# Kernel tuning notes

Hardware: AMD Instinct MI355X
Metric: run time of the kernel (lower is better)

The kernel has to match this reference:

```python
import jax, jax.numpy as jnp
import numpy as np
import math

H = 1024      # hidden_size
NH = 16       # num_attention_heads
HD = H // NH  # head_dim = 64
FF = 4096     # intermediate_size
AD = 256      # adapter_hidden_size
NB = 320      # num_buckets
MAXD = 800    # max_bucket_distance
B = 4
S = 1024
EPS = 1e-5


def _rel_bucket(rel):
    # HF WavLM _relative_positions_bucket
    nb = NB // 2
    buckets = (rel > 0).astype(jnp.int32) * nb
    rel = jnp.abs(rel)
    max_exact = nb // 2
    is_small = rel < max_exact
    large = max_exact + (
        jnp.log(jnp.maximum(rel, 1).astype(jnp.float32) / max_exact)
        / math.log(MAXD / max_exact) * (nb - max_exact)
    ).astype(jnp.int32)
    large = jnp.minimum(large, nb - 1)
    return buckets + jnp.where(is_small, rel, large)


def _ln(x, g, b):
    m = x.mean(-1, keepdims=True)
    v = ((x - m) ** 2).mean(-1, keepdims=True)
    return (x - m) * jax.lax.rsqrt(v + EPS) * g + b


def setup_inputs() -> dict:
    key = jax.random.key(0)
    ks = jax.random.split(key, 12)
    sc = 0.02
    w = lambda k, shape: jax.random.normal(k, shape, jnp.float32) * sc
    return dict(
        x=jax.random.normal(ks[0], (B, S, H), jnp.float32),
        Wq=w(ks[1], (H, H)), bq=jnp.zeros((H,), jnp.float32),
        Wk=w(ks[2], (H, H)), bk=jnp.zeros((H,), jnp.float32),
        Wv=w(ks[3], (H, H)), bv=jnp.zeros((H,), jnp.float32),
        Wo=w(ks[4], (H, H)), bo=jnp.zeros((H,), jnp.float32),
        Wg=w(ks[5], (8, HD)), bg=jnp.zeros((8,), jnp.float32),
        gru_const=jnp.ones((1, NH, 1, 1), jnp.float32),
        rel_embed=w(ks[6], (NB, NH)),
        ln1_g=jnp.ones((H,), jnp.float32), ln1_b=jnp.zeros((H,), jnp.float32),
        W1=w(ks[7], (FF, H)), b1=jnp.zeros((FF,), jnp.float32),
        W2=w(ks[8], (H, FF)), b2=jnp.zeros((H,), jnp.float32),
        ln2_g=jnp.ones((H,), jnp.float32), ln2_b=jnp.zeros((H,), jnp.float32),
        Wad=w(ks[9], (AD, H)), bad=jnp.zeros((AD,), jnp.float32),
        Wau=w(ks[10], (H, AD)), bau=jnp.zeros((H,), jnp.float32),
    )


def reference(x, Wq, bq, Wk, bk, Wv, bv, Wo, bo, Wg, bg, gru_const, rel_embed,
              ln1_g, ln1_b, W1, b1, W2, b2, ln2_g, ln2_b, Wad, bad, Wau, bau):
    b, s, _ = x.shape
    # --- relative position bias (first layer: position_bias=None) ---
    pos = jnp.arange(s)
    rel = pos[None, :] - pos[:, None]                 # memory - context
    pos_bias = rel_embed[_rel_bucket(rel)].transpose(2, 0, 1)  # (nh, s, s)

    # --- GRU-style gating of the bias (per batch, head, query pos) ---
    xh = x.reshape(b, s, NH, HD).transpose(0, 2, 1, 3)         # (b, nh, s, hd)
    gproj = jnp.einsum('bhsd,ed->bhse', xh, Wg) + bg           # (b, nh, s, 8)
    gproj = gproj.reshape(b, NH, s, 2, 4).sum(-1)              # (b, nh, s, 2)
    gate = jax.nn.sigmoid(gproj)
    gate_a, gate_b = gate[..., 0:1], gate[..., 1:2]            # (b, nh, s, 1)
    gate_out = gate_a * (gate_b * gru_const - 1.0) + 2.0       # (b, nh, s, 1)
    gated_bias = gate_out * pos_bias[None]                     # (b, nh, s, s)

    # --- multi-head self-attention with additive gated bias ---
    q = (x @ Wq.T + bq).reshape(b, s, NH, HD)
    k = (x @ Wk.T + bk).reshape(b, s, NH, HD)
    v = (x @ Wv.T + bv).reshape(b, s, NH, HD)
    scores = jnp.einsum('bihd,bjhd->bhij', q, k) * (HD ** -0.5) + gated_bias
    attn = jax.nn.softmax(scores, axis=-1)
    ctx = jnp.einsum('bhij,bjhd->bihd', attn, v).reshape(b, s, H)
    attn_out = ctx @ Wo.T + bo

    # --- residual + LN, FFN + adapter (idx_without_adapter=None path) + LN ---
    h = _ln(x + attn_out, ln1_g, ln1_b)
    ff = jax.nn.gelu(h @ W1.T + b1, approximate=False) @ W2.T + b2
    adapt = jax.nn.elu(h @ Wad.T + bad) @ Wau.T + bau
    h = h + ff + adapt
    return _ln(h, ln2_g, ln2_b)
```

## Files before the change

kernel.cpp:

```cpp
#include <hip/hip_runtime.h>
#include <cmath>

typedef unsigned short u16;
using short8 = __attribute__((ext_vector_type(8))) short;
using f32x4  = __attribute__((ext_vector_type(4))) float;

__device__ __forceinline__ u16 f2bf(float f) {
  union { float f; unsigned u; } c; c.f = f;
  unsigned r = c.u + 0x7fffu + ((c.u >> 16) & 1u);
  return (u16)(r >> 16);
}
__device__ __forceinline__ float bf2f(u16 b) {
  union { unsigned u; float f; } c; c.u = ((unsigned)b) << 16;
  return c.f;
}

__device__ __forceinline__ void gld_lds16(void* lds, const void* g) {
  __builtin_amdgcn_global_load_lds(
      (const __attribute__((address_space(1))) void*)g,
      (__attribute__((address_space(3))) void*)lds, 16, 0, 0);
}

__device__ __forceinline__ float gelu_fast(float t) {
  float u = 0.7978845608f * t * (1.f + 0.044715f * t * t);
  float th = 1.f - 2.f / (__expf(2.f * u) + 1.f);
  return 0.5f * t * (1.f + th);
}

__global__ __launch_bounds__(256) void cvt_bf16(const float* __restrict__ in,
                                                u16* __restrict__ out, int n4) {
  int i = blockIdx.x * 256 + threadIdx.x;
  if (i >= n4) return;
  float4 v = ((const float4*)in)[i];
  ushort4 o;
  o.x = f2bf(v.x); o.y = f2bf(v.y); o.z = f2bf(v.z); o.w = f2bf(v.w);
  ((ushort4*)out)[i] = o;
}

__global__ __launch_bounds__(256) void cvt_pad(const float* __restrict__ in,
                                               u16* __restrict__ out,
                                               int incols4, int outstride, int n4) {
  int i = blockIdx.x * 256 + threadIdx.x;
  if (i >= n4) return;
  int row = i / incols4, c = i - row * incols4;
  float4 v = ((const float4*)in)[i];
  ushort4 o;
  o.x = f2bf(v.x); o.y = f2bf(v.y); o.z = f2bf(v.z); o.w = f2bf(v.w);
  *(ushort4*)&out[(size_t)row * outstride + c * 4] = o;
}

__global__ __launch_bounds__(256) void btab_kernel(const float* __restrict__ rel_embed,
                                                   float* __restrict__ btab) {
  int idx = blockIdx.x * 256 + threadIdx.x;
  if (idx >= 16 * 2048) return;
  int h = idx >> 11;
  int d = idx & 2047;
  if (d >= 2047) return;
  int rel = d - 1023;
  int bucket = (rel > 0) ? 160 : 0;
  int ar = rel < 0 ? -rel : rel;
  if (ar < 80) {
    bucket += ar;
  } else {
    int large = 80 + (int)(logf((float)ar / 80.0f) / 2.3025851f * 80.0f);
    if (large > 159) large = 159;
    bucket += large;
  }
  btab[h * 2048 + d] = rel_embed[bucket * 16 + h];
}

__global__ __launch_bounds__(256) void gate_kernel(const float* __restrict__ x,
                                                   const float* __restrict__ Wg,
                                                   const float* __restrict__ bg,
                                                   const float* __restrict__ gc,
                                                   float* __restrict__ gate_out) {
  int gw = blockIdx.x * 4 + (threadIdx.x >> 6);
  int lane = threadIdx.x & 63;
  int s = gw & 1023, bh = gw >> 10, b = bh >> 4, h = bh & 15;
  float wA = Wg[lane] + Wg[64 + lane] + Wg[128 + lane] + Wg[192 + lane];
  float wB = Wg[256 + lane] + Wg[320 + lane] + Wg[384 + lane] + Wg[448 + lane];
  float xv = x[((size_t)(b * 1024 + s)) * 1024 + h * 64 + lane];
  float pa = xv * wA, pb = xv * wB;
  #pragma unroll
  for (int m = 1; m < 64; m <<= 1) {
    pa += __shfl_xor(pa, m, 64);
    pb += __shfl_xor(pb, m, 64);
  }
  if (lane == 0) {
    float bgA = bg[0] + bg[1] + bg[2] + bg[3];
    float bgB = bg[4] + bg[5] + bg[6] + bg[7];
    float ga = 1.f / (1.f + expf(-(pa + bgA)));
    float gb = 1.f / (1.f + expf(-(pb + bgB)));
    gate_out[(size_t)bh * 1024 + s] = ga * (gb * gc[h] - 1.f) + 2.f;
  }
}

__global__ __launch_bounds__(256) void vtrans_kernel(const u16* __restrict__ vb,
                                                     u16* __restrict__ vt) {
  __shared__ u16 tile[64 * 65];
  int bh = blockIdx.y, b = bh >> 4, h = bh & 15;
  int s0 = blockIdx.x * 64;
  int tid = threadIdx.x;
  int r = tid >> 3, c = (tid & 7) * 8;
  #pragma unroll
  for (int p = 0; p < 2; ++p) {
    int s = p * 32 + r;
    uint4 vv = *(const uint4*)&vb[((size_t)(b * 1024 + s0 + s)) * 1024 + h * 64 + c];
    const u16* pv = (const u16*)&vv;
    #pragma unroll
    for (int e = 0; e < 8; ++e) tile[(c + e) * 65 + s] = pv[e];
  }
  __syncthreads();
  int d = tid & 63, jc0 = tid >> 6;
  #pragma unroll
  for (int jc = jc0; jc < 8; jc += 4) {
    u16 tmp[8];
    #pragma unroll
    for (int e = 0; e < 8; ++e) tmp[e] = tile[d * 65 + jc * 8 + e];
    *(uint4*)&vt[((size_t)(bh * 64 + d)) * 1024 + s0 + jc * 8] = *(uint4*)tmp;
  }
}

template <int MODE>
__global__ __launch_bounds__(256, 3) void gemm_bt(
    const u16* __restrict__ A, const u16* __restrict__ Bw,
    int K, int Ksub, int N, int bn0,
    const float* __restrict__ bias0, const float* __restrict__ bias1,
    const float* __restrict__ bias2,
    float* __restrict__ outf,
    u16* __restrict__ ob0, u16* __restrict__ ob1, u16* __restrict__ ob2) {
  __shared__ __align__(16) u16 As[3][128 * 32];
  __shared__ __align__(16) u16 Bs[3][128 * 32];
  const int tid = threadIdx.x;
  const int lane = tid & 63, wave = tid >> 6;
  const int quad = lane >> 4, l16 = lane & 15;
  const int bm = blockIdx.x * 128, bn = blockIdx.y * 128;
  const int kz = blockIdx.z;
  const int nsteps = Ksub >> 5;
  const int wm = (wave & 1) * 64, wn = (wave >> 1) * 64;
  const int sr = lane & 15, skc = (lane >> 4) * 8;

  const u16* a0 = A + (size_t)(bm + wave * 32 + sr) * K + kz * Ksub + skc;
  const u16* b0 = Bw + (size_t)(bn + wave * 32 + sr) * K + kz * Ksub + skc;
  const size_t ra = (size_t)16 * K;

  f32x4 acc[4][4] = {};

  #pragma unroll
  for (int t = 0; t < 2; ++t) {
    gld_lds16(&As[0][(wave * 2 + t) * 512], a0 + t * ra);
    gld_lds16(&Bs[0][(wave * 2 + t) * 512], b0 + t * ra);
  }
  if (nsteps > 1) {
    #pragma unroll
    for (int t = 0; t < 2; ++t) {
      gld_lds16(&As[1][(wave * 2 + t) * 512], a0 + t * ra + 32);
      gld_lds16(&Bs[1][(wave * 2 + t) * 512], b0 + t * ra + 32);
    }
  }

  int cur = 0, nxt2 = 2;
  for (int ks = 0; ks < nsteps; ++ks) {
    if (ks + 1 < nsteps) asm volatile("s_waitcnt vmcnt(4)" ::: "memory");
    else                 asm volatile("s_waitcnt vmcnt(0)" ::: "memory");
    __builtin_amdgcn_s_barrier();
    if (ks + 2 < nsteps) {
      int ko = (ks + 2) * 32;
      #pragma unroll
      for (int t = 0; t < 2; ++t) {
        gld_lds16(&As[nxt2][(wave * 2 + t) * 512], a0 + t * ra + ko);
        gld_lds16(&Bs[nxt2][(wave * 2 + t) * 512], b0 + t * ra + ko);
      }
    }
    const u16* Ap = As[cur];
    const u16* Bp = Bs[cur];
    short8 af[4], bf[4];
    #pragma unroll
    for (int mi = 0; mi < 4; ++mi)
      af[mi] = *(const short8*)&Ap[((wm >> 4) + mi) * 512 + quad * 128 + l16 * 8];
    #pragma unroll
    for (int ni = 0; ni < 4; ++ni)
      bf[ni] = *(const short8*)&Bp[((wn >> 4) + ni) * 512 + quad * 128 + l16 * 8];
    #pragma unroll
    for (int mi = 0; mi < 4; ++mi)
      #pragma unroll
      for (int ni = 0; ni < 4; ++ni)
        acc[mi][ni] = __builtin_amdgcn_mfma_f32_16x16x32_bf16(af[mi], bf[ni], acc[mi][ni], 0, 0, 0);
    cur = (cur == 2) ? 0 : cur + 1;
    nxt2 = (nxt2 == 2) ? 0 : nxt2 + 1;
  }

  float* outp = outf + (size_t)kz * 4194304;

  #pragma unroll
  for (int mi = 0; mi < 4; ++mi) {
    #pragma unroll
    for (int ni = 0; ni < 4; ++ni) {
      int col = bn + bn0 + wn + ni * 16 + l16;
      #pragma unroll
      for (int r = 0; r < 4; ++r) {
        int m = bm + wm + mi * 16 + quad * 4 + r;
        float v = acc[mi][ni][r];
        if constexpr (MODE == 0) {
          int seg = col >> 10;
          int nloc = col & 1023;
          const float* bs = seg == 0 ? bias0 : (seg == 1 ? bias1 : bias2);
          u16* dst = seg == 0 ? ob0 : (seg == 1 ? ob1 : ob2);
          v += bs[nloc];
          if (seg == 0) v *= 0.125f;
          dst[(size_t)m * 1024 + nloc] = f2bf(v);
        } else if constexpr (MODE == 2) {
          if (col < 4096) {
            float t = v + bias0[col];
            ob0[(size_t)m * 4352 + col] = f2bf(gelu_fast(t));
          } else {
            float t = v + bias1[col - 4096];
            float e = t > 0.f ? t : (__expf(t) - 1.f);
            ob0[(size_t)m * 4352 + col] = f2bf(e);
          }
        } else {
          outp[(size_t)m * N + col] = v;
        }
      }
    }
  }
}

#define VMCNT(n) asm volatile("s_waitcnt vmcnt(" #n ")" ::: "memory")
#define NOOPST ((void)0)

#define G256_LDA(BUF, KK, MH)                                               \
  af_[0] = *(const short8*)&lds[BUF][0][KK][aBase + (MH) * 2048 + 0];       \
  af_[1] = *(const short8*)&lds[BUF][0][KK][aBase + (MH) * 2048 + 512];     \
  af_[2] = *(const short8*)&lds[BUF][0][KK][aBase + (MH) * 2048 + 1024];    \
  af_[3] = *(const short8*)&lds[BUF][0][KK][aBase + (MH) * 2048 + 1536];
#define G256_LDB(BUF, KK)                                                   \
  bf_[0] = *(const short8*)&lds[BUF][1][KK][bBase + 0];                     \
  bf_[1] = *(const short8*)&lds[BUF][1][KK][bBase + 512];                   \
  bf_[2] = *(const short8*)&lds[BUF][1][KK][bBase + 1024];                  \
  bf_[3] = *(const short8*)&lds[BUF][1][KK][bBase + 1536];
#define G256_MFMA(MH)                                                       \
  _Pragma("unroll") for (int mi = 0; mi < 4; ++mi)                          \
  _Pragma("unroll") for (int ni = 0; ni < 4; ++ni)                          \
    acc[(MH) * 4 + mi][ni] = __builtin_amdgcn_mfma_f32_16x16x32_bf16(       \
        af_[mi], bf_[ni], acc[(MH) * 4 + mi][ni], 0, 0, 0);
#define G256_PHASE(BUF, KK, MH, DOB, STAGE, WAIT)                           \
  {                                                                         \
    G256_LDA(BUF, KK, MH)                                                   \
    if (DOB) { G256_LDB(BUF, KK) }                                          \
    STAGE;                                                                  \
    __builtin_amdgcn_s_barrier();                                           \
    asm volatile("s_waitcnt lgkmcnt(0)" ::: "memory");                      \
    __builtin_amdgcn_s_setprio(1);                                          \
    G256_MFMA(MH)                                                           \
    __builtin_amdgcn_s_setprio(0);                                          \
    WAIT;                                                                   \
    __builtin_amdgcn_s_barrier();                                           \
  }

template <int MODE>
__global__ __launch_bounds__(512, 2) void gemm256(
    const u16* __restrict__ A, const u16* __restrict__ Bw,
    int lda, int ldb, int kt_hi, int kt_lo, int z_hi,
    const float* __restrict__ bias0, const float* __restrict__ bias1,
    const float* __restrict__ bias2,
    float* __restrict__ outf, float* __restrict__ outf2, int ldo,
    u16* __restrict__ ob0, u16* __restrict__ ob1, u16* __restrict__ ob2) {
  __shared__ __align__(16) u16 lds[2][2][2][8192];

  const int tid = threadIdx.x;
  const int lane = tid & 63, wave = tid >> 6;
  const int quad = lane >> 4, l16 = lane & 15;
  const int wm = wave >> 2, wn = wave & 3;

  const int gx = gridDim.x, gy = gridDim.y;
  int flat = blockIdx.x + gx * (blockIdx.y + gy * blockIdx.z);
  const int cpx = (gx * gy * gridDim.z) >> 3;
  flat = (flat & 7) * cpx + (flat >> 3);
  const int bmi = flat % gx;
  int rest = flat / gx;
  const int bni = rest % gy;
  const int kz = rest / gy;

  const int bm = bmi * 256, bn = bni * 256;
  const int nkt = (kz < z_hi) ? kt_hi : kt_lo;
  const int ktb = (kz < z_hi) ? kz * kt_hi : z_hi * kt_hi + (kz - z_hi) * kt_lo;
  const int nIter = nkt >> 1;

  const int srow = wave * 16 + (lane >> 2);
  const int sk = (((lane & 3) ^ ((lane >> 3) & 3)) << 3);
  const u16* aG = A + (size_t)(bm + srow) * lda + (size_t)ktb * 64 + sk;
  const u16* bG = Bw + (size_t)(bn + srow) * ldb + (size_t)ktb * 64 + sk;
  const size_t aS = (size_t)128 * lda, bS = (size_t)128 * ldb;

  const int xsw = ((quad ^ ((l16 >> 1) & 3)) << 3);
  const int aBase = (wm * 128 + l16) * 32 + xsw;
  const int bBase = (wn * 64 + l16) * 32 + xsw;

  auto stA = [&](int buf, int kh, int kt) {
    const u16* g = aG + kt * 64 + kh * 32;
    u16* d = (u16*)&lds[buf][0][kh][wave * 512];
    gld_lds16(d, g);
    gld_lds16(d + 4096, g + aS);
  };
  auto stB = [&](int buf, int kh, int kt) {
    const u16* g = bG + kt * 64 + kh * 32;
    u16* d = (u16*)&lds[buf][1][kh][wave * 512];
    gld_lds16(d, g);
    gld_lds16(d + 4096, g + bS);
  };

  f32x4 acc[8][4] = {};
  short8 af_[4], bf_[4];

  stA(0, 0, 0); stB(0, 0, 0); stA(0, 1, 0); stB(0, 1, 0);
  stA(1, 0, 1); stB(1, 0, 1);
  VMCNT(0);
  __builtin_amdgcn_s_barrier();

  for (int J = 0; J < nIter - 1; ++J) {
    const int o = 2 * J + 1, e = 2 * J + 2, on = 2 * J + 3;
    G256_PHASE(0, 0, 0, 1, stA(1, 1, o),  NOOPST)
    G256_PHASE(0, 0, 1, 0, stB(1, 1, o),  VMCNT(8))
    G256_PHASE(0, 1, 0, 1, stA(0, 0, e),  NOOPST)
    G256_PHASE(0, 1, 1, 0, stB(0, 0, e),  VMCNT(8))
    G256_PHASE(1, 0, 0, 1, stA(0, 1, e),  NOOPST)
    G256_PHASE(1, 0, 1, 0, stB(0, 1, e),  VMCNT(8))
    G256_PHASE(1, 1, 0, 1, stA(1, 0, on), NOOPST)
    G256_PHASE(1, 1, 1, 0, stB(1, 0, on), VMCNT(8))
  }
  {
    const int o = nkt - 1;
    G256_PHASE(0, 0, 0, 1, stA(1, 1, o), NOOPST)
    G256_PHASE(0, 0, 1, 0, stB(1, 1, o), NOOPST)
    G256_PHASE(0, 1, 0, 1, NOOPST,       NOOPST)
    G256_PHASE(0, 1, 1, 0, NOOPST,       VMCNT(4))
    G256_PHASE(1, 0, 0, 1, NOOPST,       NOOPST)
    G256_PHASE(1, 0, 1, 0, NOOPST,       VMCNT(0))
    G256_PHASE(1, 1, 0, 1, NOOPST,       NOOPST)
    G256_PHASE(1, 1, 1, 0, NOOPST,       NOOPST)
  }

  const int m0 = bm + wm * 128 + quad * 4;
  const int n0 = bn + wn * 64 + l16;

  if constexpr (MODE == 0) {
    const int seg = bn >> 10;
    const float* bs = seg == 0 ? bias0 : (seg == 1 ? bias1 : bias2);
    u16* dst = seg == 0 ? ob0 : (seg == 1 ? ob1 : ob2);
    const float sc = seg == 0 ? 0.125f : 1.0f;
    const int nb = (bn & 1023) + wn * 64 + l16;
    #pragma unroll
    for (int a = 0; a < 8; ++a)
      #pragma unroll
      for (int ni = 0; ni < 4; ++ni) {
        int nn = nb + ni * 16;
        float bv = bs[nn];
        #pragma unroll
        for (int r = 0; r < 4; ++r) {
          int m = m0 + a * 16 + r;
          dst[(size_t)m * 1024 + nn] = f2bf((acc[a][ni][r] + bv) * sc);
        }
      }
  } else if constexpr (MODE == 2) {
    #pragma unroll
    for (int a = 0; a < 8; ++a)
      #pragma unroll
      for (int ni = 0; ni < 4; ++ni) {
        int nn = n0 + ni * 16;
        float bv = bias0[nn];
        #pragma unroll
        for (int r = 0; r < 4; ++r) {
          int m = m0 + a * 16 + r;
          ob0[(size_t)m * 4352 + nn] = f2bf(gelu_fast(acc[a][ni][r] + bv));
        }
      }
  } else {
    float* op = (kz < 2) ? outf + (size_t)kz * 4194304
                         : outf2 + (size_t)(kz - 2) * 4194304;
    #pragma unroll
    for (int a = 0; a < 8; ++a)
      #pragma unroll
      for (int ni = 0; ni < 4; ++ni) {
        int nn = n0 + ni * 16;
        #pragma unroll
        for (int r = 0; r < 4; ++r)
          op[(size_t)(m0 + a * 16 + r) * ldo + nn] = acc[a][ni][r];
      }
  }
}

__global__ __launch_bounds__(256) void attn_kernel(
    const u16* __restrict__ qb, const u16* __restrict__ kb, const u16* __restrict__ vt,
    const float* __restrict__ gate, const float* __restrict__ btab,
    u16* __restrict__ ctxb) {
  __shared__ __align__(16) u16 Qs[64 * 64];
  __shared__ __align__(16) u16 Ks[64 * 64];
  __shared__ __align__(16) u16 Vs[64 * 64];
  __shared__ __align__(16) u16 Ps[4][16 * 64];
  __shared__ u16 btl[2048];
  __shared__ float gbuf[64];

  const int tid = threadIdx.x;
  const int lane = tid & 63, wave = tid >> 6;
  const int quad = lane >> 4, l16 = lane & 15;
  const int it0 = blockIdx.x * 64;
  const int bh = blockIdx.y, b = bh >> 4, h = bh & 15;
  const int sr = lane & 15;
  const int skc = (lane >> 4) * 8;

  for (int idx = tid; idx < 2047; idx += 256) btl[idx] = f2bf(btab[h * 2048 + idx]);
  if (tid < 64) gbuf[tid] = gate[(size_t)bh * 1024 + it0 + tid];

  #pragma unroll
  for (int hf = 0; hf < 2; ++hf)
    gld_lds16(&Qs[wave * 1024 + hf * 512],
              &qb[((size_t)(b * 1024 + it0 + wave * 16 + sr)) * 1024 + h * 64 + hf * 32 + skc]);

  f32x4 oacc[4] = {};
  float mrow[4], lrow[4];
  #pragma unroll
  for (int r = 0; r < 4; ++r) { mrow[r] = -1e30f; lrow[r] = 0.f; }

  __syncthreads();

  for (int jt = 0; jt < 16; ++jt) {
    int j0 = jt * 64;
    #pragma unroll
    for (int hf = 0; hf < 2; ++hf) {
      gld_lds16(&Ks[wave * 1024 + hf * 512],
                &kb[((size_t)(b * 1024 + j0 + wave * 16 + sr)) * 1024 + h * 64 + hf * 32 + skc]);
      gld_lds16(&Vs[wave * 1024 + hf * 512],
                &vt[((size_t)(bh * 64 + wave * 16 + sr)) * 1024 + j0 + hf * 32 + skc]);
    }
    __syncthreads();

    f32x4 sacc[4] = {};
    #pragma unroll
    for (int c = 0; c < 2; ++c) {
      short8 aq = *(const short8*)&Qs[wave * 1024 + (c * 4 + quad) * 128 + l16 * 8];
      #pragma unroll
      for (int nt = 0; nt < 4; ++nt) {
        short8 bk8 = *(const short8*)&Ks[nt * 1024 + (c * 4 + quad) * 128 + l16 * 8];
        sacc[nt] = __builtin_amdgcn_mfma_f32_16x16x32_bf16(aq, bk8, sacc[nt], 0, 0, 0);
      }
    }

    float sc[4][4], mt[4];
    #pragma unroll
    for (int r = 0; r < 4; ++r) {
      int i_loc = wave * 16 + quad * 4 + r;
      int i_glob = it0 + i_loc;
      float g = gbuf[i_loc];
      float mx = -1e30f;
      #pragma unroll
      for (int nt = 0; nt < 4; ++nt) {
        int j = j0 + nt * 16 + l16;
        float s = sacc[nt][r] + g * bf2f(btl[j - i_glob + 1023]);
        sc[nt][r] = s;
        mx = fmaxf(mx, s);
      }
      mt[r] = mx;
    }
    #pragma unroll
    for (int m = 1; m < 16; m <<= 1)
      #pragma unroll
      for (int r = 0; r < 4; ++r) mt[r] = fmaxf(mt[r], __shfl_xor(mt[r], m, 64));

    float alpha[4], ls[4];
    #pragma unroll
    for (int r = 0; r < 4; ++r) {
      float mnew = fmaxf(mrow[r], mt[r]);
      alpha[r] = __expf(mrow[r] - mnew);
      mrow[r] = mnew;
      float lsum = 0.f;
      #pragma unroll
      for (int nt = 0; nt < 4; ++nt) {
        float p = __expf(sc[nt][r] - mnew);
        sc[nt][r] = p;
        lsum += p;
      }
      ls[r] = lsum;
    }
    #pragma unroll
    for (int m = 1; m < 16; m <<= 1)
      #pragma unroll
      for (int r = 0; r < 4; ++r) ls[r] += __shfl_xor(ls[r], m, 64);
    #pragma unroll
    for (int r = 0; r < 4; ++r) lrow[r] = lrow[r] * alpha[r] + ls[r];

    #pragma unroll
    for (int nt = 0; nt < 4; ++nt)
      #pragma unroll
      for (int r = 0; r < 4; ++r)
        Ps[wave][(nt * 2 + (l16 >> 3)) * 128 + (quad * 4 + r) * 8 + (l16 & 7)] = f2bf(sc[nt][r]);

    #pragma unroll
    for (int dt = 0; dt < 4; ++dt)
      #pragma unroll
      for (int r = 0; r < 4; ++r) oacc[dt][r] *= alpha[r];

    #pragma unroll
    for (int c = 0; c < 2; ++c) {
      short8 ap = *(const short8*)&Ps[wave][(c * 4 + quad) * 128 + l16 * 8];
      #pragma unroll
      for (int dt = 0; dt < 4; ++dt) {
        short8 bv8 = *(const short8*)&Vs[dt * 1024 + (c * 4 + quad) * 128 + l16 * 8];
        oacc[dt] = __builtin_amdgcn_mfma_f32_16x16x32_bf16(ap, bv8, oacc[dt], 0, 0, 0);
      }
    }
    __syncthreads();
  }

  #pragma unroll
  for (int dt = 0; dt < 4; ++dt)
    #pragma unroll
    for (int r = 0; r < 4; ++r) {
      int i_loc = wave * 16 + quad * 4 + r;
      int d = dt * 16 + l16;
      float o = oacc[dt][r] / lrow[r];
      ctxb[((size_t)(b * 1024 + it0 + i_loc)) * 1024 + h * 64 + d] = f2bf(o);
    }
}

template <bool WRITE_BF16, bool TWO_BIAS, int NP>
__global__ __launch_bounds__(256) void redln_kernel(
    const float* __restrict__ p0, const float* __restrict__ p1,
    const float* __restrict__ p2, const float* __restrict__ p3,
    const float* __restrict__ extra, const float* __restrict__ bias,
    const float* __restrict__ bias2,
    const float* __restrict__ g, const float* __restrict__ bta,
    float* __restrict__ outf, u16* __restrict__ outb) {
  __shared__ float red[8];
  int row = blockIdx.x, tid = threadIdx.x;
  int lane = tid & 63, wave = tid >> 6;
  size_t base = (size_t)row * 1024 + tid * 4;
  float4 a = *(const float4*)&p0[base];
  float4 bb = *(const float4*)&p1[base];
  float4 c = *(const float4*)&extra[base];
  float4 d = *(const float4*)&bias[tid * 4];
  float4 v;
  v.x = a.x + bb.x + c.x + d.x;
  v.y = a.y + bb.y + c.y + d.y;
  v.z = a.z + bb.z + c.z + d.z;
  v.w = a.w + bb.w + c.w + d.w;
  if (NP == 4) {
    float4 e2 = *(const float4*)&p2[base];
    float4 e3 = *(const float4*)&p3[base];
    v.x += e2.x + e3.x; v.y += e2.y + e3.y;
    v.z += e2.z + e3.z; v.w += e2.w + e3.w;
  }
  if (TWO_BIAS) {
    float4 d2 = *(const float4*)&bias2[tid * 4];
    v.x += d2.x; v.y += d2.y; v.z += d2.z; v.w += d2.w;
  }
  float s = v.x + v.y + v.z + v.w;
  #pragma unroll
  for (int m = 1; m < 64; m <<= 1) s += __shfl_xor(s, m, 64);
  if (lane == 0) red[wave] = s;
  __syncthreads();
  float mean = (red[0] + red[1] + red[2] + red[3]) * (1.f / 1024.f);
  float d0 = v.x - mean, d1 = v.y - mean, d2 = v.z - mean, d3 = v.w - mean;
  float sq = d0 * d0 + d1 * d1 + d2 * d2 + d3 * d3;
  #pragma unroll
  for (int m = 1; m < 64; m <<= 1) sq += __shfl_xor(sq, m, 64);
  if (lane == 0) red[4 + wave] = sq;
  __syncthreads();
  float var = (red[4] + red[5] + red[6] + red[7]) * (1.f / 1024.f);
  float rstd = rsqrtf(var + 1e-5f);
  float dd[4] = {d0, d1, d2, d3};
  #pragma unroll
  for (int e = 0; e < 4; ++e) {
    int cidx = tid * 4 + e;
    float val = dd[e] * rstd * g[cidx] + bta[cidx];
    outf[(size_t)row * 1024 + cidx] = val;
    if (WRITE_BF16) outb[(size_t)row * 1024 + cidx] = f2bf(val);
  }
}

extern "C" void kernel_launch(void* const* d_in, const int* in_sizes, int n_in,
                              void* d_out, int out_size, void* d_ws, size_t ws_size,
                              hipStream_t stream) {
  const float* x    = (const float*)d_in[0];
  const float* Wq   = (const float*)d_in[1];  const float* bq  = (const float*)d_in[2];
  const float* Wk   = (const float*)d_in[3];  const float* bk  = (const float*)d_in[4];
  const float* Wv   = (const float*)d_in[5];  const float* bv  = (const float*)d_in[6];
  const float* Wo   = (const float*)d_in[7];  const float* bo  = (const float*)d_in[8];
  const float* Wg   = (const float*)d_in[9];  const float* bg  = (const float*)d_in[10];
  const float* gc   = (const float*)d_in[11];
  const float* rel  = (const float*)d_in[12];
  const float* ln1g = (const float*)d_in[13]; const float* ln1b = (const float*)d_in[14];
  const float* W1   = (const float*)d_in[15]; const float* b1  = (const float*)d_in[16];
  const float* W2   = (const float*)d_in[17]; const float* b2  = (const float*)d_in[18];
  const float* ln2g = (const float*)d_in[19]; const float* ln2b = (const float*)d_in[20];
  const float* Wad  = (const float*)d_in[21]; const float* bad = (const float*)d_in[22];
  const float* Wau  = (const float*)d_in[23]; const float* bau = (const float*)d_in[24];
  float* out = (float*)d_out;

  char* ws = (char*)d_ws;
  const size_t MB = 1ull << 20;
  const size_t KB = 1ull << 10;
  (void)n_in; (void)in_sizes; (void)out_size;

  const bool big = ws_size >= (135ull << 20);

  u16 *xb, *wqkv, *qb, *kb, *vbp, *vtb, *ctxb, *wob, *w1ad, *w2au, *ffadp, *hb;
  float *gate, *btab, *P0, *P1, *P2, *P3, *hf;
  xb    = (u16*)(ws + 0 * MB);
  wqkv  = (u16*)(ws + 8 * MB);
  ffadp = (u16*)(ws + 0 * MB);
  P0    = (float*)(ws + 34 * MB);
  P1    = (float*)(ws + 50 * MB);
  if (big) {
    P2   = (float*)(ws + 66 * MB);
    P3   = (float*)(ws + 82 * MB);
    qb   = (u16*)(ws + 66 * MB);
    kb   = (u16*)(ws + 74 * MB);
    vbp  = (u16*)(ws + 82 * MB);
    vtb  = (u16*)(ws + 90 * MB);
    hb   = (u16*)(ws + 82 * MB);
    ctxb = (u16*)(ws + 98 * MB);
    hf   = (float*)(ws + 98 * MB);
    wob  = (u16*)(ws + 114 * MB);
    w1ad = (u16*)(ws + 116 * MB);
    w2au = (u16*)(ws + 125 * MB);
    gate = (float*)(ws + 133 * MB + 512 * KB);
    btab = (float*)(ws + 133 * MB + 768 * KB);
  } else {
    P2   = P0;  P3 = P0;
    qb   = (u16*)(ws + 14 * MB);
    kb   = (u16*)(ws + 22 * MB);
    vbp  = (u16*)(ws + 30 * MB);
    vtb  = (u16*)(ws + 38 * MB);
    gate = (float*)(ws + 46 * MB);
    btab = (float*)(ws + 46 * MB + 256 * KB);
    ctxb = (u16*)(ws + 66 * MB);
    wob  = (u16*)(ws + 74 * MB);
    w1ad = (u16*)(ws + 76 * MB);
    w2au = (u16*)(ws + 85 * MB);
    hf   = (float*)(ws + 94 * MB);
    hb   = (u16*)(ws + 110 * MB);
  }

  auto cvt = [&](const float* src, u16* dst, int n) {
    cvt_bf16<<<(n / 4 + 255) / 256, 256, 0, stream>>>(src, dst, n / 4);
  };
  cvt(x, xb, 4096 * 1024);
  cvt(Wq, wqkv,               1024 * 1024);
  cvt(Wk, wqkv + 1024 * 1024, 1024 * 1024);
  cvt(Wv, wqkv + 2 * 1024 * 1024, 1024 * 1024);
  cvt(Wo, wob, 1024 * 1024);
  cvt(W1, w1ad, 4096 * 1024);
  cvt(Wad, w1ad + 4096 * 1024, 256 * 1024);
  cvt_pad<<<(1024 * 1024 + 255) / 256, 256, 0, stream>>>(W2, w2au, 1024, 4352, 1024 * 1024);
  cvt_pad<<<(64 * 1024 + 255) / 256, 256, 0, stream>>>(Wau, w2au + 4096, 64, 4352, 64 * 1024);

  btab_kernel<<<128, 256, 0, stream>>>(rel, btab);
  gate_kernel<<<16384, 256, 0, stream>>>(x, Wg, bg, gc, gate);

  gemm256<0><<<dim3(16, 12, 1), 512, 0, stream>>>(xb, wqkv, 1024, 1024, 16, 16, 1,
      bq, bk, bv, nullptr, nullptr, 0, qb, kb, vbp);
  vtrans_kernel<<<dim3(16, 64), 256, 0, stream>>>(vbp, vtb);
  attn_kernel<<<dim3(16, 64), 256, 0, stream>>>(qb, kb, vtb, gate, btab, ctxb);
  gemm_bt<3><<<dim3(32, 8, 2), 256, 0, stream>>>(ctxb, wob, 1024, 512, 1024, 0,
      nullptr, nullptr, nullptr, P0, nullptr, nullptr, nullptr);
  redln_kernel<true, false, 2><<<4096, 256, 0, stream>>>(P0, P1, P0, P0, x, bo, nullptr,
      ln1g, ln1b, hf, hb);
  gemm256<2><<<dim3(16, 16, 1), 512, 0, stream>>>(hb, w1ad, 1024, 1024, 16, 16, 1,
      b1, nullptr, nullptr, nullptr, nullptr, 0, ffadp, nullptr, nullptr);
  gemm_bt<2><<<dim3(32, 2, 1), 256, 0, stream>>>(hb, w1ad + 4096 * 1024, 1024, 1024, 4352,
      4096, bad, bad, nullptr, nullptr, ffadp, nullptr, nullptr);
  if (big) {
    gemm256<3><<<dim3(16, 4, 4), 512, 0, stream>>>(ffadp, w2au, 4352, 4352, 18, 16, 2,
        nullptr, nullptr, nullptr, P0, P2, 1024, nullptr, nullptr, nullptr);
    redln_kernel<false, true, 4><<<4096, 256, 0, stream>>>(P0, P1, P2, P3, hf, b2, bau,
        ln2g, ln2b, out, nullptr);
  } else {
    gemm256<3><<<dim3(16, 4, 2), 512, 0, stream>>>(ffadp, w2au, 4352, 4352, 34, 34, 2,
        nullptr, nullptr, nullptr, P0, P2, 1024, nullptr, nullptr, nullptr);
    redln_kernel<false, true, 2><<<4096, 256, 0, stream>>>(P0, P1, P0, P0, hf, b2, bau,
        ln2g, ln2b, out, nullptr);
  }
}
```

Baseline: 548.8 us.

## Simplify GEMM pipeline, drop attention LDS staging, fuse adapter into FFN GEMM

The 256-tile GEMM drops its fine-grained 8-phase ping-pong schedule and instead issues a whole next-tile prefetch, computes the current tile, then waits with vmcnt(0) and one barrier per tile. The attention kernel no longer stages Q/K/V through LDS and reads the operands straight from global memory into registers, which removes its per-iteration syncthreads. The adapter down-projection is folded into the FFN-up GEMM by adding a 17th column block with an ELU epilogue, and the small-workspace path now always uses the 4-way split-K W2 GEMM. These changes cut barriers and launches, but they lose the fine-grained overlap of loads with MFMA work and rely on uncached-style global loads inside attention.

Result: faster. 536.8 us (-2.2%).

```diff
diff --git a/kernel.cpp b/kernel.cpp
--- a/kernel.cpp
+++ b/kernel.cpp
@@ -227,7 +227,6 @@
 }
 
 #define VMCNT(n) asm volatile("s_waitcnt vmcnt(" #n ")" ::: "memory")
-#define NOOPST ((void)0)
 
 #define G256_LDA(BUF, KK, MH)                                               \
   af_[0] = *(const short8*)&lds[BUF][0][KK][aBase + (MH) * 2048 + 0];       \
@@ -244,19 +243,17 @@
   _Pragma("unroll") for (int ni = 0; ni < 4; ++ni)                          \
     acc[(MH) * 4 + mi][ni] = __builtin_amdgcn_mfma_f32_16x16x32_bf16(       \
         af_[mi], bf_[ni], acc[(MH) * 4 + mi][ni], 0, 0, 0);
-#define G256_PHASE(BUF, KK, MH, DOB, STAGE, WAIT)                           \
-  {                                                                         \
-    G256_LDA(BUF, KK, MH)                                                   \
-    if (DOB) { G256_LDB(BUF, KK) }                                          \
-    STAGE;                                                                  \
-    __builtin_amdgcn_s_barrier();                                           \
-    asm volatile("s_waitcnt lgkmcnt(0)" ::: "memory");                      \
-    __builtin_amdgcn_s_setprio(1);                                          \
-    G256_MFMA(MH)                                                           \
-    __builtin_amdgcn_s_setprio(0);                                          \
-    WAIT;                                                                   \
-    __builtin_amdgcn_s_barrier();                                           \
-  }
+#define G256_TILE(BUF)                                                      \
+  G256_LDB(BUF, 0)                                                          \
+  G256_LDA(BUF, 0, 0)                                                       \
+  G256_MFMA(0)                                                              \
+  G256_LDA(BUF, 0, 1)                                                       \
+  G256_MFMA(1)                                                              \
+  G256_LDB(BUF, 1)                                                          \
+  G256_LDA(BUF, 1, 0)                                                       \
+  G256_MFMA(0)                                                              \
+  G256_LDA(BUF, 1, 1)                                                       \
+  G256_MFMA(1)
 
 template <int MODE>
 __global__ __launch_bounds__(512, 2) void gemm256(
@@ -285,7 +282,6 @@
   const int bm = bmi * 256, bn = bni * 256;
   const int nkt = (kz < z_hi) ? kt_hi : kt_lo;
   const int ktb = (kz < z_hi) ? kz * kt_hi : z_hi * kt_hi + (kz - z_hi) * kt_lo;
-  const int nIter = nkt >> 1;
 
   const int srow = wave * 16 + (lane >> 2);
   const int sk = (((lane & 3) ^ ((lane >> 3) & 3)) << 3);
@@ -314,31 +310,24 @@
   short8 af_[4], bf_[4];
 
   stA(0, 0, 0); stB(0, 0, 0); stA(0, 1, 0); stB(0, 1, 0);
-  stA(1, 0, 1); stB(1, 0, 1);
   VMCNT(0);
   __builtin_amdgcn_s_barrier();
 
-  for (int J = 0; J < nIter - 1; ++J) {
-    const int o = 2 * J + 1, e = 2 * J + 2, on = 2 * J + 3;
-    G256_PHASE(0, 0, 0, 1, stA(1, 1, o),  NOOPST)
-    G256_PHASE(0, 0, 1, 0, stB(1, 1, o),  VMCNT(8))
-    G256_PHASE(0, 1, 0, 1, stA(0, 0, e),  NOOPST)
-    G256_PHASE(0, 1, 1, 0, stB(0, 0, e),  VMCNT(8))
-    G256_PHASE(1, 0, 0, 1, stA(0, 1, e),  NOOPST)
-    G256_PHASE(1, 0, 1, 0, stB(0, 1, e),  VMCNT(8))
-    G256_PHASE(1, 1, 0, 1, stA(1, 0, on), NOOPST)
-    G256_PHASE(1, 1, 1, 0, stB(1, 0, on), VMCNT(8))
-  }
-  {
-    const int o = nkt - 1;
-    G256_PHASE(0, 0, 0, 1, stA(1, 1, o), NOOPST)
-    G256_PHASE(0, 0, 1, 0, stB(1, 1, o), NOOPST)
-    G256_PHASE(0, 1, 0, 1, NOOPST,       NOOPST)
-    G256_PHASE(0, 1, 1, 0, NOOPST,       VMCNT(4))
-    G256_PHASE(1, 0, 0, 1, NOOPST,       NOOPST)
-    G256_PHASE(1, 0, 1, 0, NOOPST,       VMCNT(0))
-    G256_PHASE(1, 1, 0, 1, NOOPST,       NOOPST)
-    G256_PHASE(1, 1, 1, 0, NOOPST,       NOOPST)
+  for (int J = 0; J < (nkt >> 1); ++J) {
+    {
+      const int t1 = 2 * J + 1;
+      stA(1, 0, t1); stB(1, 0, t1); stA(1, 1, t1); stB(1, 1, t1);
+      G256_TILE(0)
+      VMCNT(0);
+      __builtin_amdgcn_s_barrier();
+    }
+    {
+      const int t2 = 2 * J + 2;
+      if (t2 < nkt) { stA(0, 0, t2); stB(0, 0, t2); stA(0, 1, t2); stB(0, 1, t2); }
+      G256_TILE(1)
+      VMCNT(0);
+      __builtin_amdgcn_s_barrier();
+    }
   }
 
   const int m0 = bm + wm * 128 + quad * 4;
@@ -363,16 +352,21 @@
         }
       }
   } else if constexpr (MODE == 2) {
+    const bool is_gelu = (bn < 4096);
     #pragma unroll
     for (int a = 0; a < 8; ++a)
       #pragma unroll
       for (int ni = 0; ni < 4; ++ni) {
         int nn = n0 + ni * 16;
-        float bv = bias0[nn];
+        float bv = is_gelu ? bias0[nn] : bias1[nn - 4096];
         #pragma unroll
         for (int r = 0; r < 4; ++r) {
           int m = m0 + a * 16 + r;
-          ob0[(size_t)m * 4352 + nn] = f2bf(gelu_fast(acc[a][ni][r] + bv));
+          float t = acc[a][ni][r] + bv;
+          float res;
+          if (is_gelu) res = gelu_fast(t);
+          else         res = t > 0.f ? t : (__expf(t) - 1.f);
+          ob0[(size_t)m * 4352 + nn] = f2bf(res);
         }
       }
   } else {
@@ -394,9 +388,6 @@
     const u16* __restrict__ qb, const u16* __restrict__ kb, const u16* __restrict__ vt,
     const float* __restrict__ gate, const float* __restrict__ btab,
     u16* __restrict__ ctxb) {
-  __shared__ __align__(16) u16 Qs[64 * 64];
-  __shared__ __align__(16) u16 Ks[64 * 64];
-  __shared__ __align__(16) u16 Vs[64 * 64];
   __shared__ __align__(16) u16 Ps[4][16 * 64];
   __shared__ u16 btl[2048];
   __shared__ float gbuf[64];
@@ -406,16 +397,15 @@
   const int quad = lane >> 4, l16 = lane & 15;
   const int it0 = blockIdx.x * 64;
   const int bh = blockIdx.y, b = bh >> 4, h = bh & 15;
-  const int sr = lane & 15;
-  const int skc = (lane >> 4) * 8;
 
   for (int idx = tid; idx < 2047; idx += 256) btl[idx] = f2bf(btab[h * 2048 + idx]);
   if (tid < 64) gbuf[tid] = gate[(size_t)bh * 1024 + it0 + tid];
 
-  #pragma unroll
-  for (int hf = 0; hf < 2; ++hf)
-    gld_lds16(&Qs[wave * 1024 + hf * 512],
-              &qb[((size_t)(b * 1024 + it0 + wave * 16 + sr)) * 1024 + h * 64 + hf * 32 + skc]);
+  short8 aq[2];
+  #pragma unroll
+  for (int c = 0; c < 2; ++c)
+    aq[c] = *(const short8*)&qb[((size_t)(b * 1024 + it0 + wave * 16 + l16)) * 1024 +
+                                h * 64 + c * 32 + quad * 8];
 
   f32x4 oacc[4] = {};
   float mrow[4], lrow[4];
@@ -425,26 +415,25 @@
   __syncthreads();
 
   for (int jt = 0; jt < 16; ++jt) {
-    int j0 = jt * 64;
-    #pragma unroll
-    for (int hf = 0; hf < 2; ++hf) {
-      gld_lds16(&Ks[wave * 1024 + hf * 512],
-                &kb[((size_t)(b * 1024 + j0 + wave * 16 + sr)) * 1024 + h * 64 + hf * 32 + skc]);
-      gld_lds16(&Vs[wave * 1024 + hf * 512],
-                &vt[((size_t)(bh * 64 + wave * 16 + sr)) * 1024 + j0 + hf * 32 + skc]);
-    }
-    __syncthreads();
+    const int j0 = jt * 64;
 
     f32x4 sacc[4] = {};
     #pragma unroll
-    for (int c = 0; c < 2; ++c) {
-      short8 aq = *(const short8*)&Qs[wave * 1024 + (c * 4 + quad) * 128 + l16 * 8];
+    for (int c = 0; c < 2; ++c)
       #pragma unroll
       for (int nt = 0; nt < 4; ++nt) {
-        short8 bk8 = *(const short8*)&Ks[nt * 1024 + (c * 4 + quad) * 128 + l16 * 8];
-        sacc[nt] = __builtin_amdgcn_mfma_f32_16x16x32_bf16(aq, bk8, sacc[nt], 0, 0, 0);
-      }
-    }
+        short8 bk8 = *(const short8*)&kb[((size_t)(b * 1024 + j0 + nt * 16 + l16)) * 1024 +
+                                         h * 64 + c * 32 + quad * 8];
+        sacc[nt] = __builtin_amdgcn_mfma_f32_16x16x32_bf16(aq[c], bk8, sacc[nt], 0, 0, 0);
+      }
+
+    short8 bv[2][4];
+    #pragma unroll
+    for (int c = 0; c < 2; ++c)
+      #pragma unroll
+      for (int dt = 0; dt < 4; ++dt)
+        bv[c][dt] = *(const short8*)&vt[((size_t)(bh * 64 + dt * 16 + l16)) * 1024 +
+                                        j0 + c * 32 + quad * 8];
 
     float sc[4][4], mt[4];
     #pragma unroll
@@ -504,12 +493,9 @@
     for (int c = 0; c < 2; ++c) {
       short8 ap = *(const short8*)&Ps[wave][(c * 4 + quad) * 128 + l16 * 8];
       #pragma unroll
-      for (int dt = 0; dt < 4; ++dt) {
-        short8 bv8 = *(const short8*)&Vs[dt * 1024 + (c * 4 + quad) * 128 + l16 * 8];
-        oacc[dt] = __builtin_amdgcn_mfma_f32_16x16x32_bf16(ap, bv8, oacc[dt], 0, 0, 0);
-      }
-    }
-    __syncthreads();
+      for (int dt = 0; dt < 4; ++dt)
+        oacc[dt] = __builtin_amdgcn_mfma_f32_16x16x32_bf16(ap, bv[c][dt], oacc[dt], 0, 0, 0);
+    }
   }
 
   #pragma unroll
@@ -627,7 +613,6 @@
     gate = (float*)(ws + 133 * MB + 512 * KB);
     btab = (float*)(ws + 133 * MB + 768 * KB);
   } else {
-    P2   = P0;  P3 = P0;
     qb   = (u16*)(ws + 14 * MB);
     kb   = (u16*)(ws + 22 * MB);
     vbp  = (u16*)(ws + 30 * MB);
@@ -640,6 +625,8 @@
     w2au = (u16*)(ws + 85 * MB);
     hf   = (float*)(ws + 94 * MB);
     hb   = (u16*)(ws + 110 * MB);
+    P2   = (float*)(ws + 66 * MB);
+    P3   = (float*)(ws + 14 * MB);
   }
 
   auto cvt = [&](const float* src, u16* dst, int n) {
@@ -666,19 +653,10 @@
       nullptr, nullptr, nullptr, P0, nullptr, nullptr, nullptr);
   redln_kernel<true, false, 2><<<4096, 256, 0, stream>>>(P0, P1, P0, P0, x, bo, nullptr,
       ln1g, ln1b, hf, hb);
-  gemm256<2><<<dim3(16, 16, 1), 512, 0, stream>>>(hb, w1ad, 1024, 1024, 16, 16, 1,
-      b1, nullptr, nullptr, nullptr, nullptr, 0, ffadp, nullptr, nullptr);
-  gemm_bt<2><<<dim3(32, 2, 1), 256, 0, stream>>>(hb, w1ad + 4096 * 1024, 1024, 1024, 4352,
-      4096, bad, bad, nullptr, nullptr, ffadp, nullptr, nullptr);
-  if (big) {
-    gemm256<3><<<dim3(16, 4, 4), 512, 0, stream>>>(ffadp, w2au, 4352, 4352, 18, 16, 2,
-        nullptr, nullptr, nullptr, P0, P2, 1024, nullptr, nullptr, nullptr);
-    redln_kernel<false, true, 4><<<4096, 256, 0, stream>>>(P0, P1, P2, P3, hf, b2, bau,
-        ln2g, ln2b, out, nullptr);
-  } else {
-    gemm256<3><<<dim3(16, 4, 2), 512, 0, stream>>>(ffadp, w2au, 4352, 4352, 34, 34, 2,
-        nullptr, nullptr, nullptr, P0, P2, 1024, nullptr, nullptr, nullptr);
-    redln_kernel<false, true, 2><<<4096, 256, 0, stream>>>(P0, P1, P0, P0, hf, b2, bau,
-        ln2g, ln2b, out, nullptr);
-  }
-}
+  gemm256<2><<<dim3(16, 17, 1), 512, 0, stream>>>(hb, w1ad, 1024, 1024, 16, 16, 1,
+      b1, bad, nullptr, nullptr, nullptr, 0, ffadp, nullptr, nullptr);
+  gemm256<3><<<dim3(16, 4, 4), 512, 0, stream>>>(ffadp, w2au, 4352, 4352, 18, 16, 2,
+      nullptr, nullptr, nullptr, P0, P2, 1024, nullptr, nullptr, nullptr);
+  redln_kernel<false, true, 4><<<4096, 256, 0, stream>>>(P0, P1, P2, P3, hf, b2, bau,
+      ln2g, ln2b, out, nullptr);
+}
```
